# Kernel optimization log

Measured on AMD Instinct MI355X. Metric: run time of the kernel, lower is better.

## Reference

```python
import jax, jax.numpy as jnp
import numpy as np

TAU = 2.0
V_TH = 1.0


def setup_inputs() -> dict:
    key = jax.random.key(0)
    k1, k2, k3 = jax.random.split(key, 3)
    T, B, H = 128, 64, 1024
    x = jax.random.normal(k1, (T, B, H), dtype=jnp.float32)
    # nn.Linear(H, H, bias=False) weights, shape [out, in]
    W1 = jax.random.normal(k2, (H, H), dtype=jnp.float32) / np.sqrt(H)
    W2 = jax.random.normal(k3, (H, H), dtype=jnp.float32) / np.sqrt(H)
    return {"x": x, "W1": W1, "W2": W2}


def _lif_scan(x_proj):
    # x_proj: [T, B, H]; membrane v starts at 0.
    def step(v, xt):
        h = v + (xt - v) / TAU          # leaky integrate
        s = (h >= V_TH).astype(h.dtype)  # hard-threshold spike
        v_new = h * (1.0 - s)            # soft reset (to 0 on spike)
        return v_new, s

    v0 = jnp.zeros(x_proj.shape[1:], dtype=x_proj.dtype)
    _, spikes = jax.lax.scan(step, v0, x_proj)
    return spikes  # [T, B, H]


def reference(x, W1, W2):
    # fc1 applied per timestep == one batched GEMM over [T*B, H]
    x_proj = jnp.einsum('tbh,oh->tbo', x, W1)
    spike = _lif_scan(x_proj)
    out = jnp.einsum('tbh,oh->tbo', spike, W2)
    return out
```

## Files before the change

### kernel.cpp

```cpp
#include <hip/hip_runtime.h>
#include <hip/hip_bf16.h>
#include <stdint.h>

#define TT 128
#define BB 64
#define HH 1024
#define MM (TT * BB)
#define NLANE (BB * HH)
#define DELTA 1.0e-4
#define F16_ONE 0x3C00

typedef __attribute__((ext_vector_type(8))) short bf16x8;
typedef __attribute__((ext_vector_type(8))) _Float16 f16x8;
typedef __attribute__((ext_vector_type(4))) float f32x4;

#define GLOAD16(g, l)                                                        \
    __builtin_amdgcn_global_load_lds(                                        \
        (const __attribute__((address_space(1))) unsigned int*)(g),          \
        (__attribute__((address_space(3))) unsigned int*)(l), 16, 0, 0)

static __device__ __forceinline__ unsigned short bf16_bits(float f) {
    __hip_bfloat16 b = __float2bfloat16(f);
    return *reinterpret_cast<unsigned short*>(&b);
}
static __device__ __forceinline__ unsigned short f16_bits(float f) {
    _Float16 h = (_Float16)f;
    return *reinterpret_cast<unsigned short*>(&h);
}

__global__ __launch_bounds__(256) void prep_fused(const float* __restrict__ x,
                                                  const float* __restrict__ W1,
                                                  const float* __restrict__ W2,
                                                  unsigned short* __restrict__ Xhi,
                                                  unsigned short* __restrict__ Xlo,
                                                  unsigned short* __restrict__ W1hi,
                                                  unsigned short* __restrict__ W1lo,
                                                  unsigned short* __restrict__ w2h,
                                                  int* __restrict__ cnt) {
    const int bid = blockIdx.x;
    if (bid == 0 && threadIdx.x == 0) *cnt = 0;

    const float* src;
    unsigned short *hi, *lo;
    int i;
    bool split;
    if (bid < 8192) {
        i = bid * 256 + threadIdx.x;
        src = x; hi = Xhi; lo = Xlo; split = true;
    } else if (bid < 9216) {
        i = (bid - 8192) * 256 + threadIdx.x;
        src = W1; hi = W1hi; lo = W1lo; split = true;
    } else {
        i = (bid - 9216) * 256 + threadIdx.x;
        src = W2; hi = w2h; lo = nullptr; split = false;
    }

    float4 v4 = reinterpret_cast<const float4*>(src)[i];
    float v[4] = {v4.x, v4.y, v4.z, v4.w};
    unsigned short hb[4], lb[4];
#pragma unroll
    for (int c = 0; c < 4; c++) {
        if (split) {
            hb[c] = bf16_bits(v[c]);
            __hip_bfloat16 hh = *reinterpret_cast<__hip_bfloat16*>(&hb[c]);
            lb[c] = bf16_bits(v[c] - __bfloat162float(hh));
        } else {
            hb[c] = f16_bits(v[c]);
        }
    }
    reinterpret_cast<ushort4*>(hi)[i] = make_ushort4(hb[0], hb[1], hb[2], hb[3]);
    if (split)
        reinterpret_cast<ushort4*>(lo)[i] = make_ushort4(lb[0], lb[1], lb[2], lb[3]);
}

__global__ __launch_bounds__(256) void gemm1_mfma(const unsigned short* __restrict__ Ah,
                                                  const unsigned short* __restrict__ Al,
                                                  const unsigned short* __restrict__ Bh,
                                                  const unsigned short* __restrict__ Bl,
                                                  float* __restrict__ C) {
    __shared__ short AsH[128 * 32];
    __shared__ short AsL[128 * 32];
    __shared__ short BsH[128 * 32];
    __shared__ short BsL[128 * 32];

    const int tid = threadIdx.x;
    const int lane = tid & 63;
    const int wave = tid >> 6;
    const int m0 = blockIdx.x * 128;
    const int n0 = blockIdx.y * 128;
    const int wm = (wave >> 1) * 64;
    const int wn = (wave & 1) * 64;

    const int rsel = lane & 15;
    const int part = lane >> 4;

    int adrA[4], adrB[4];
#pragma unroll
    for (int i = 0; i < 4; i++) {
        const int ra = wm + i * 16 + rsel;
        const int rb = wn + i * 16 + rsel;
        adrA[i] = ra * 32 + (part ^ ((ra >> 1) & 3)) * 8;
        adrB[i] = rb * 32 + (part ^ ((rb >> 1) & 3)) * 8;
    }

    f32x4 acc[4][4] = {};

    for (int k0 = 0; k0 < HH; k0 += 32) {
#pragma unroll
        for (int p = 0; p < 2; p++) {
            const int c = tid + p * 256;
            const int cb = wave * 64 + p * 256;
            const int row = c >> 2;
            const int pslot = c & 3;
            const int pdata = pslot ^ ((row >> 1) & 3);
            const size_t goA = (size_t)(m0 + row) * HH + k0 + pdata * 8;
            const size_t goB = (size_t)(n0 + row) * HH + k0 + pdata * 8;
            GLOAD16(&Ah[goA], &AsH[cb * 8]);
            GLOAD16(&Al[goA], &AsL[cb * 8]);
            GLOAD16(&Bh[goB], &BsH[cb * 8]);
            GLOAD16(&Bl[goB], &BsL[cb * 8]);
        }
        __syncthreads();

        bf16x8 aH[4], aL[4], bH[4], bL[4];
#pragma unroll
        for (int mi = 0; mi < 4; mi++) {
            aH[mi] = *reinterpret_cast<bf16x8*>(&AsH[adrA[mi]]);
            aL[mi] = *reinterpret_cast<bf16x8*>(&AsL[adrA[mi]]);
        }
#pragma unroll
        for (int ni = 0; ni < 4; ni++) {
            bH[ni] = *reinterpret_cast<bf16x8*>(&BsH[adrB[ni]]);
            bL[ni] = *reinterpret_cast<bf16x8*>(&BsL[adrB[ni]]);
        }

#pragma unroll
        for (int mi = 0; mi < 4; mi++)
#pragma unroll
            for (int ni = 0; ni < 4; ni++) {
                acc[mi][ni] = __builtin_amdgcn_mfma_f32_16x16x32_bf16(aH[mi], bH[ni], acc[mi][ni], 0, 0, 0);
                acc[mi][ni] = __builtin_amdgcn_mfma_f32_16x16x32_bf16(aH[mi], bL[ni], acc[mi][ni], 0, 0, 0);
                acc[mi][ni] = __builtin_amdgcn_mfma_f32_16x16x32_bf16(aL[mi], bH[ni], acc[mi][ni], 0, 0, 0);
            }

        __syncthreads();
    }

    const int col = lane & 15;
    const int quad = lane >> 4;
#pragma unroll
    for (int mi = 0; mi < 4; mi++)
#pragma unroll
        for (int ni = 0; ni < 4; ni++) {
            const int m = m0 + wm + mi * 16 + quad * 4;
            const int n = n0 + wn + ni * 16 + col;
            float* dst = &C[(size_t)m * HH + n];
#pragma unroll
            for (int r = 0; r < 4; r++)
                dst[(size_t)r * HH] = acc[mi][ni][r];
        }
}

__global__ __launch_bounds__(256) void lif_scan_flag(const float* __restrict__ xp,
                                                     unsigned short* __restrict__ sp,
                                                     int* __restrict__ count,
                                                     int* __restrict__ list) {
    const int idx = blockIdx.x * 256 + threadIdx.x;
    double v = 0.0;
    bool flg = false;
#pragma unroll 4
    for (int t = 0; t < TT; t++) {
        const double x = (double)xp[(size_t)t * NLANE + idx];
        const double h = v + (x - v) * 0.5;
        const bool s = (h >= 1.0);
        flg |= (fabs(h - 1.0) < DELTA);
        v = s ? 0.0 : h;
        sp[(size_t)t * NLANE + idx] = s ? (unsigned short)F16_ONE : (unsigned short)0;
    }
    if (flg) {
        const int i = atomicAdd(count, 1);
        list[i] = idx;
    }
}

__global__ __launch_bounds__(1024) void recompute_fused(const float* __restrict__ X,
                                                        const float* __restrict__ W1,
                                                        const int* __restrict__ count,
                                                        const int* __restrict__ list,
                                                        unsigned short* __restrict__ sp) {
    __shared__ double hbuf[TT];
    const int cnt = *count;
    const int wv = threadIdx.x >> 6;
    const int ln = threadIdx.x & 63;

    for (int li = blockIdx.x; li < cnt; li += gridDim.x) {
        const int lane = list[li];
        const int b = lane >> 10;
        const int h = lane & (HH - 1);
        const float4* w4 = reinterpret_cast<const float4*>(W1 + (size_t)h * HH);

        for (int t = wv; t < TT; t += 16) {
            const float4* x4 = reinterpret_cast<const float4*>(X + (size_t)(t * BB + b) * HH);
            double s0 = 0.0, s1 = 0.0, s2 = 0.0, s3 = 0.0;
#pragma unroll
            for (int i = 0; i < 4; i++) {
                const float4 xa = x4[ln + i * 64];
                const float4 wa = w4[ln + i * 64];
                s0 = fma((double)xa.x, (double)wa.x, s0);
                s1 = fma((double)xa.y, (double)wa.y, s1);
                s2 = fma((double)xa.z, (double)wa.z, s2);
                s3 = fma((double)xa.w, (double)wa.w, s3);
            }
            double s = (s0 + s1) + (s2 + s3);
#pragma unroll
            for (int off = 32; off >= 1; off >>= 1)
                s += __shfl_down(s, off);
            if (ln == 0) hbuf[t] = s;
        }
        __syncthreads();

        if (threadIdx.x == 0) {
            double v = 0.0;
            for (int t = 0; t < TT; t++) {
                const double hh = v + (hbuf[t] - v) * 0.5;
                const bool s = (hh >= 1.0);
                v = s ? 0.0 : hh;
                sp[(size_t)t * NLANE + lane] = s ? (unsigned short)F16_ONE : (unsigned short)0;
            }
        }
        __syncthreads();
    }
}

__global__ __launch_bounds__(256) void gemm2_mfma(const unsigned short* __restrict__ S,
                                                  const unsigned short* __restrict__ W,
                                                  float* __restrict__ O) {
    __shared__ short As[128 * 32];
    __shared__ short Bs[64 * 32];

    const int tid = threadIdx.x;
    const int lane = tid & 63;
    const int wave = tid >> 6;
    const int m0 = blockIdx.y * 128;
    const int n0 = blockIdx.x * 64;
    const int wm = (wave >> 1) * 64;
    const int wn = (wave & 1) * 32;

    const int rsel = lane & 15;
    const int part = lane >> 4;

    int adrA[4], adrB[2];
#pragma unroll
    for (int i = 0; i < 4; i++) {
        const int ra = wm + i * 16 + rsel;
        adrA[i] = ra * 32 + (part ^ ((ra >> 1) & 3)) * 8;
    }
#pragma unroll
    for (int i = 0; i < 2; i++) {
        const int rb = wn + i * 16 + rsel;
        adrB[i] = rb * 32 + (part ^ ((rb >> 1) & 3)) * 8;
    }

    f32x4 acc[4][2] = {};

    for (int k0 = 0; k0 < HH; k0 += 32) {
#pragma unroll
        for (int p = 0; p < 3; p++) {
            const int c = tid + p * 256;
            const int cb = wave * 64 + p * 256;
            if (c < 512) {
                const int row = c >> 2;
                const int pslot = c & 3;
                const int pdata = pslot ^ ((row >> 1) & 3);
                GLOAD16(&S[(size_t)(m0 + row) * HH + k0 + pdata * 8], &As[cb * 8]);
            } else {
                const int c2 = c - 512;
                const int row = c2 >> 2;
                const int pslot = c2 & 3;
                const int pdata = pslot ^ ((row >> 1) & 3);
                GLOAD16(&W[(size_t)(n0 + row) * HH + k0 + pdata * 8], &Bs[(cb - 512) * 8]);
            }
        }
        __syncthreads();

        f16x8 a[4], b[2];
#pragma unroll
        for (int mi = 0; mi < 4; mi++)
            a[mi] = *reinterpret_cast<f16x8*>(&As[adrA[mi]]);
#pragma unroll
        for (int ni = 0; ni < 2; ni++)
            b[ni] = *reinterpret_cast<f16x8*>(&Bs[adrB[ni]]);

#pragma unroll
        for (int mi = 0; mi < 4; mi++)
#pragma unroll
            for (int ni = 0; ni < 2; ni++)
                acc[mi][ni] = __builtin_amdgcn_mfma_f32_16x16x32_f16(
                    a[mi], b[ni], acc[mi][ni], 0, 0, 0);

        __syncthreads();
    }

    const int col = lane & 15;
    const int quad = lane >> 4;
#pragma unroll
    for (int mi = 0; mi < 4; mi++)
#pragma unroll
        for (int ni = 0; ni < 2; ni++) {
            const int m = m0 + wm + mi * 16 + quad * 4;
            const int n = n0 + wn + ni * 16 + col;
            float* dst = &O[(size_t)m * HH + n];
#pragma unroll
            for (int r = 0; r < 4; r++)
                dst[(size_t)r * HH] = acc[mi][ni][r];
        }
}

extern "C" void kernel_launch(void* const* d_in, const int* in_sizes, int n_in,
                              void* d_out, int out_size, void* d_ws, size_t ws_size,
                              hipStream_t stream) {
    const float* x  = (const float*)d_in[0];
    const float* W1 = (const float*)d_in[1];
    const float* W2 = (const float*)d_in[2];
    float* out = (float*)d_out;

    char* ws = (char*)d_ws;
    const size_t szX = (size_t)MM * HH;
    const size_t szW = (size_t)HH * HH;

    unsigned short* Xhi  = (unsigned short*)ws;
    unsigned short* Xlo  = Xhi + szX;
    unsigned short* W1hi = Xlo + szX;
    unsigned short* W1lo = W1hi + szW;
    unsigned short* w2h  = W1lo + szW;
    int*            list = (int*)(w2h + szW);
    int*            cnt  = list + NLANE;
    float*          xp   = (float*)(((uintptr_t)(cnt + 64) + 255) & ~(uintptr_t)255);
    unsigned short* sp   = Xhi;

    prep_fused<<<10240, 256, 0, stream>>>(x, W1, W2, Xhi, Xlo, W1hi, W1lo, w2h, cnt);

    dim3 g1(MM / 128, HH / 128);
    gemm1_mfma<<<g1, 256, 0, stream>>>(Xhi, Xlo, W1hi, W1lo, xp);

    lif_scan_flag<<<NLANE / 256, 256, 0, stream>>>(xp, sp, cnt, list);

    recompute_fused<<<512, 1024, 0, stream>>>(x, W1, cnt, list, sp);

    dim3 g2(HH / 64, MM / 128);
    gemm2_mfma<<<g2, 256, 0, stream>>>(sp, w2h, out);
}
```

Measured before the change: 215.5 us.

## Rewrite split-bf16 GEMM1 as pipelined 256x128 kernel with concatenated hi/lo K

The prep kernel now writes the hi and lo bf16 halves of x and W1 side by side in each row, forming a K=2048 operand. GEMM1 becomes a 512-thread, 256x128-tile kernel that walks a 48-step K schedule covering the hi·hi, lo·hi and hi·lo products. It double-buffers LDS with global_load_lds, interleaves loads and MFMAs in phases controlled by explicit waitcnt, barriers and setprio, and remaps block IDs for L2 locality. The aim is to hide memory latency and raise MFMA utilisation. The cost is heavy manual scheduling and a larger LDS footprint.

```diff
diff --git a/kernel.cpp b/kernel.cpp
--- a/kernel.cpp
+++ b/kernel.cpp
@@ -19,6 +19,8 @@
         (const __attribute__((address_space(1))) unsigned int*)(g),          \
         (__attribute__((address_space(3))) unsigned int*)(l), 16, 0, 0)
 
+#define FENCE() __builtin_amdgcn_sched_barrier(0)
+
 static __device__ __forceinline__ unsigned short bf16_bits(float f) {
     __hip_bfloat16 b = __float2bfloat16(f);
     return *reinterpret_cast<unsigned short*>(&b);
@@ -31,129 +33,183 @@
 __global__ __launch_bounds__(256) void prep_fused(const float* __restrict__ x,
                                                   const float* __restrict__ W1,
                                                   const float* __restrict__ W2,
-                                                  unsigned short* __restrict__ Xhi,
-                                                  unsigned short* __restrict__ Xlo,
-                                                  unsigned short* __restrict__ W1hi,
-                                                  unsigned short* __restrict__ W1lo,
+                                                  unsigned short* __restrict__ A2,
+                                                  unsigned short* __restrict__ B2,
                                                   unsigned short* __restrict__ w2h,
                                                   int* __restrict__ cnt) {
     const int bid = blockIdx.x;
     if (bid == 0 && threadIdx.x == 0) *cnt = 0;
 
-    const float* src;
-    unsigned short *hi, *lo;
-    int i;
-    bool split;
-    if (bid < 8192) {
-        i = bid * 256 + threadIdx.x;
-        src = x; hi = Xhi; lo = Xlo; split = true;
-    } else if (bid < 9216) {
-        i = (bid - 8192) * 256 + threadIdx.x;
-        src = W1; hi = W1hi; lo = W1lo; split = true;
-    } else {
-        i = (bid - 9216) * 256 + threadIdx.x;
-        src = W2; hi = w2h; lo = nullptr; split = false;
-    }
-
-    float4 v4 = reinterpret_cast<const float4*>(src)[i];
-    float v[4] = {v4.x, v4.y, v4.z, v4.w};
-    unsigned short hb[4], lb[4];
-#pragma unroll
-    for (int c = 0; c < 4; c++) {
-        if (split) {
+    if (bid < 9216) {
+        const bool isX = (bid < 8192);
+        const int i = (isX ? bid : bid - 8192) * 256 + threadIdx.x;
+        const float4 v4 = reinterpret_cast<const float4*>(isX ? x : W1)[i];
+        float v[4] = {v4.x, v4.y, v4.z, v4.w};
+        unsigned short hb[4], lb[4];
+#pragma unroll
+        for (int c = 0; c < 4; c++) {
             hb[c] = bf16_bits(v[c]);
             __hip_bfloat16 hh = *reinterpret_cast<__hip_bfloat16*>(&hb[c]);
             lb[c] = bf16_bits(v[c] - __bfloat162float(hh));
-        } else {
-            hb[c] = f16_bits(v[c]);
-        }
-    }
-    reinterpret_cast<ushort4*>(hi)[i] = make_ushort4(hb[0], hb[1], hb[2], hb[3]);
-    if (split)
-        reinterpret_cast<ushort4*>(lo)[i] = make_ushort4(lb[0], lb[1], lb[2], lb[3]);
-}
-
-__global__ __launch_bounds__(256) void gemm1_mfma(const unsigned short* __restrict__ Ah,
-                                                  const unsigned short* __restrict__ Al,
-                                                  const unsigned short* __restrict__ Bh,
-                                                  const unsigned short* __restrict__ Bl,
-                                                  float* __restrict__ C) {
-    __shared__ short AsH[128 * 32];
-    __shared__ short AsL[128 * 32];
-    __shared__ short BsH[128 * 32];
-    __shared__ short BsL[128 * 32];
+        }
+        ushort4* dst = reinterpret_cast<ushort4*>(isX ? A2 : B2);
+        const int r = i >> 8;
+        const int c4 = i & 255;
+        dst[(size_t)r * 512 + c4]       = make_ushort4(hb[0], hb[1], hb[2], hb[3]);
+        dst[(size_t)r * 512 + 256 + c4] = make_ushort4(lb[0], lb[1], lb[2], lb[3]);
+    } else {
+        const int i = (bid - 9216) * 256 + threadIdx.x;
+        const float4 v4 = reinterpret_cast<const float4*>(W2)[i];
+        float v[4] = {v4.x, v4.y, v4.z, v4.w};
+        unsigned short hb[4];
+#pragma unroll
+        for (int c = 0; c < 4; c++) hb[c] = f16_bits(v[c]);
+        reinterpret_cast<ushort4*>(w2h)[i] = make_ushort4(hb[0], hb[1], hb[2], hb[3]);
+    }
+}
+
+__global__ __launch_bounds__(512, 2) void gemm1_8ph(const unsigned short* __restrict__ A2,
+                                                    const unsigned short* __restrict__ B2,
+                                                    float* __restrict__ C) {
+    __shared__ short As_[2][256 * 64];
+    __shared__ short Bs_[2][128 * 64];
 
     const int tid = threadIdx.x;
     const int lane = tid & 63;
     const int wave = tid >> 6;
-    const int m0 = blockIdx.x * 128;
-    const int n0 = blockIdx.y * 128;
-    const int wm = (wave >> 1) * 64;
-    const int wn = (wave & 1) * 64;
+    const int wr = wave >> 2;
+    const int wc = wave & 3;
+
+    const int bid = blockIdx.x;
+    const int orig = (bid & 7) * 32 + (bid >> 3);
+    const int m0 = (orig >> 3) * 256;
+    const int n0 = (orig & 7) * 128;
 
     const int rsel = lane & 15;
     const int part = lane >> 4;
 
-    int adrA[4], adrB[4];
-#pragma unroll
-    for (int i = 0; i < 4; i++) {
-        const int ra = wm + i * 16 + rsel;
-        const int rb = wn + i * 16 + rsel;
-        adrA[i] = ra * 32 + (part ^ ((ra >> 1) & 3)) * 8;
-        adrB[i] = rb * 32 + (part ^ ((rb >> 1) & 3)) * 8;
-    }
-
-    f32x4 acc[4][4] = {};
-
-    for (int k0 = 0; k0 < HH; k0 += 32) {
-#pragma unroll
-        for (int p = 0; p < 2; p++) {
-            const int c = tid + p * 256;
-            const int cb = wave * 64 + p * 256;
-            const int row = c >> 2;
-            const int pslot = c & 3;
-            const int pdata = pslot ^ ((row >> 1) & 3);
-            const size_t goA = (size_t)(m0 + row) * HH + k0 + pdata * 8;
-            const size_t goB = (size_t)(n0 + row) * HH + k0 + pdata * 8;
-            GLOAD16(&Ah[goA], &AsH[cb * 8]);
-            GLOAD16(&Al[goA], &AsL[cb * 8]);
-            GLOAD16(&Bh[goB], &BsH[cb * 8]);
-            GLOAD16(&Bl[goB], &BsL[cb * 8]);
-        }
-        __syncthreads();
-
-        bf16x8 aH[4], aL[4], bH[4], bL[4];
-#pragma unroll
-        for (int mi = 0; mi < 4; mi++) {
-            aH[mi] = *reinterpret_cast<bf16x8*>(&AsH[adrA[mi]]);
-            aL[mi] = *reinterpret_cast<bf16x8*>(&AsL[adrA[mi]]);
-        }
-#pragma unroll
-        for (int ni = 0; ni < 4; ni++) {
-            bH[ni] = *reinterpret_cast<bf16x8*>(&BsH[adrB[ni]]);
-            bL[ni] = *reinterpret_cast<bf16x8*>(&BsL[adrB[ni]]);
-        }
-
-#pragma unroll
-        for (int mi = 0; mi < 4; mi++)
-#pragma unroll
-            for (int ni = 0; ni < 4; ni++) {
-                acc[mi][ni] = __builtin_amdgcn_mfma_f32_16x16x32_bf16(aH[mi], bH[ni], acc[mi][ni], 0, 0, 0);
-                acc[mi][ni] = __builtin_amdgcn_mfma_f32_16x16x32_bf16(aH[mi], bL[ni], acc[mi][ni], 0, 0, 0);
-                acc[mi][ni] = __builtin_amdgcn_mfma_f32_16x16x32_bf16(aL[mi], bH[ni], acc[mi][ni], 0, 0, 0);
+    int adrA[8][2], adrB[2][2];
+#pragma unroll
+    for (int mi = 0; mi < 8; mi++) {
+        const int ra = wr * 128 + mi * 16 + rsel;
+#pragma unroll
+        for (int ks = 0; ks < 2; ks++) {
+            const int slot = ks * 4 + part;
+            adrA[mi][ks] = ra * 64 + ((slot ^ (ra & 7)) << 3);
+        }
+    }
+#pragma unroll
+    for (int ni = 0; ni < 2; ni++) {
+        const int rb = wc * 32 + ni * 16 + rsel;
+#pragma unroll
+        for (int ks = 0; ks < 2; ks++) {
+            const int slot = ks * 4 + part;
+            adrB[ni][ks] = rb * 64 + ((slot ^ (rb & 7)) << 3);
+        }
+    }
+
+    const int srow = tid >> 3;
+    const int gslot8 = ((tid & 7) ^ (srow & 7)) << 3;
+    const int ldso = wave * 512;
+
+#define STAGE_A(buf, q, kcol)                                                     \
+    GLOAD16(&A2[(size_t)(m0 + (q) * 64 + srow) * 2048 + (kcol) + gslot8],         \
+            &As_[buf][(q) * 4096 + ldso])
+#define STAGE_B(buf, b, kcol)                                                     \
+    GLOAD16(&B2[(size_t)(n0 + (b) * 64 + srow) * 2048 + (kcol) + gslot8],         \
+            &Bs_[buf][(b) * 4096 + ldso])
+
+#define KA_OF(t) (((t) < 16) ? (t) * 64 : (t) * 64 - 1024)
+#define KB_OF(t) (((t) < 32) ? (t) * 64 : (t) * 64 - 2048)
+
+    STAGE_A(0, 0, 0); STAGE_A(0, 2, 0);
+    STAGE_B(0, 0, 0); STAGE_B(0, 1, 0);
+    STAGE_A(0, 1, 0); STAGE_A(0, 3, 0);
+    STAGE_B(1, 0, 64); STAGE_B(1, 1, 64);
+    STAGE_A(1, 0, 64); STAGE_A(1, 2, 64);
+    asm volatile("s_waitcnt vmcnt(6)" ::: "memory");
+    FENCE();
+    __builtin_amdgcn_s_barrier();
+    FENCE();
+
+    f32x4 acc[8][2] = {};
+
+    for (int t = 0; t < 48; ++t) {
+        const short* As = As_[t & 1];
+        const short* Bs = Bs_[t & 1];
+        const int t1 = t + 1, t2 = t + 2;
+        const int kA1 = KA_OF(t1);
+        const int kA2 = KA_OF(t2);
+        const int kB2 = KB_OF(t2);
+
+        bf16x8 a[4][2], b[2][2];
+
+#pragma unroll
+        for (int mi = 0; mi < 4; mi++)
+#pragma unroll
+            for (int ks = 0; ks < 2; ks++)
+                a[mi][ks] = *reinterpret_cast<const bf16x8*>(&As[adrA[mi][ks]]);
+#pragma unroll
+        for (int ni = 0; ni < 2; ni++)
+#pragma unroll
+            for (int ks = 0; ks < 2; ks++)
+                b[ni][ks] = *reinterpret_cast<const bf16x8*>(&Bs[adrB[ni][ks]]);
+        STAGE_A((t1 & 1), 1, kA1);
+        STAGE_A((t1 & 1), 3, kA1);
+        FENCE();
+        __builtin_amdgcn_s_barrier();
+        FENCE();
+        __builtin_amdgcn_s_setprio(1);
+#pragma unroll
+        for (int mi = 0; mi < 4; mi++)
+#pragma unroll
+            for (int ni = 0; ni < 2; ni++) {
+                acc[mi][ni] = __builtin_amdgcn_mfma_f32_16x16x32_bf16(a[mi][0], b[ni][0], acc[mi][ni], 0, 0, 0);
+                acc[mi][ni] = __builtin_amdgcn_mfma_f32_16x16x32_bf16(a[mi][1], b[ni][1], acc[mi][ni], 0, 0, 0);
             }
-
-        __syncthreads();
-    }
+        __builtin_amdgcn_s_setprio(0);
+        asm volatile("s_waitcnt vmcnt(6)" ::: "memory");
+        FENCE();
+        __builtin_amdgcn_s_barrier();
+        FENCE();
+
+#pragma unroll
+        for (int mi = 0; mi < 4; mi++)
+#pragma unroll
+            for (int ks = 0; ks < 2; ks++)
+                a[mi][ks] = *reinterpret_cast<const bf16x8*>(&As[adrA[mi + 4][ks]]);
+        STAGE_B((t & 1), 0, kB2);
+        STAGE_B((t & 1), 1, kB2);
+        STAGE_A((t & 1), 0, kA2);
+        STAGE_A((t & 1), 2, kA2);
+        FENCE();
+        __builtin_amdgcn_s_barrier();
+        FENCE();
+        __builtin_amdgcn_s_setprio(1);
+#pragma unroll
+        for (int mi = 0; mi < 4; mi++)
+#pragma unroll
+            for (int ni = 0; ni < 2; ni++) {
+                acc[mi + 4][ni] = __builtin_amdgcn_mfma_f32_16x16x32_bf16(a[mi][0], b[ni][0], acc[mi + 4][ni], 0, 0, 0);
+                acc[mi + 4][ni] = __builtin_amdgcn_mfma_f32_16x16x32_bf16(a[mi][1], b[ni][1], acc[mi + 4][ni], 0, 0, 0);
+            }
+        __builtin_amdgcn_s_setprio(0);
+        asm volatile("s_waitcnt vmcnt(6)" ::: "memory");
+        FENCE();
+        __builtin_amdgcn_s_barrier();
+        FENCE();
+    }
+#undef STAGE_A
+#undef STAGE_B
 
     const int col = lane & 15;
     const int quad = lane >> 4;
 #pragma unroll
-    for (int mi = 0; mi < 4; mi++)
-#pragma unroll
-        for (int ni = 0; ni < 4; ni++) {
-            const int m = m0 + wm + mi * 16 + quad * 4;
-            const int n = n0 + wn + ni * 16 + col;
+    for (int mi = 0; mi < 8; mi++)
+#pragma unroll
+        for (int ni = 0; ni < 2; ni++) {
+            const int m = m0 + wr * 128 + mi * 16 + quad * 4;
+            const int n = n0 + wc * 32 + ni * 16 + col;
             float* dst = &C[(size_t)m * HH + n];
 #pragma unroll
             for (int r = 0; r < 4; r++)
@@ -325,23 +381,18 @@
     float* out = (float*)d_out;
 
     char* ws = (char*)d_ws;
-    const size_t szX = (size_t)MM * HH;
-    const size_t szW = (size_t)HH * HH;
-
-    unsigned short* Xhi  = (unsigned short*)ws;
-    unsigned short* Xlo  = Xhi + szX;
-    unsigned short* W1hi = Xlo + szX;
-    unsigned short* W1lo = W1hi + szW;
-    unsigned short* w2h  = W1lo + szW;
-    int*            list = (int*)(w2h + szW);
+
+    unsigned short* A2   = (unsigned short*)ws;
+    unsigned short* B2   = A2 + (size_t)MM * 2048;
+    unsigned short* w2h  = B2 + (size_t)HH * 2048;
+    int*            list = (int*)(w2h + (size_t)HH * HH);
     int*            cnt  = list + NLANE;
     float*          xp   = (float*)(((uintptr_t)(cnt + 64) + 255) & ~(uintptr_t)255);
-    unsigned short* sp   = Xhi;
-
-    prep_fused<<<10240, 256, 0, stream>>>(x, W1, W2, Xhi, Xlo, W1hi, W1lo, w2h, cnt);
-
-    dim3 g1(MM / 128, HH / 128);
-    gemm1_mfma<<<g1, 256, 0, stream>>>(Xhi, Xlo, W1hi, W1lo, xp);
+    unsigned short* sp   = (unsigned short*)ws;
+
+    prep_fused<<<10240, 256, 0, stream>>>(x, W1, W2, A2, B2, w2h, cnt);
+
+    gemm1_8ph<<<256, 512, 0, stream>>>(A2, B2, xp);
 
     lif_scan_flag<<<NLANE / 256, 256, 0, stream>>>(xp, sp, cnt, list);
 
```

After: 217.4 us. Within noise of the previous version (+0.9%).
